# Kernel optimization log

Measured on AMD Instinct MI355X. Metric: run time of the kernel, lower is better.

## Reference

```python
import jax, jax.numpy as jnp
import numpy as np

EPS = 1e-06

def _pairwise_giou(pred, target):
    # pred: [B,P,4], target: [B,G,4] -> gious [B,P,G]
    p = pred[:, :, None, :]   # [B,P,1,4]
    t = target[:, None, :, :] # [B,1,G,4]
    pw = jnp.clip(p[..., 2] - p[..., 0] + 1.0, 0.0)
    ph = jnp.clip(p[..., 3] - p[..., 1] + 1.0, 0.0)
    tw = jnp.clip(t[..., 2] - t[..., 0] + 1.0, 0.0)
    th = jnp.clip(t[..., 3] - t[..., 1] + 1.0, 0.0)
    pred_areas = pw * ph
    target_areas = tw * th
    ix1 = jnp.maximum(p[..., 0], t[..., 0])
    iy1 = jnp.maximum(p[..., 1], t[..., 1])
    ix2 = jnp.minimum(p[..., 2], t[..., 2])
    iy2 = jnp.minimum(p[..., 3], t[..., 3])
    iw = jnp.clip(ix2 - ix1 + 1.0, 0.0)
    ih = jnp.clip(iy2 - iy1 + 1.0, 0.0)
    inter = iw * ih
    unions = pred_areas + target_areas - inter
    ious = jnp.maximum(inter / unions, EPS)
    ox1 = jnp.minimum(p[..., 0], t[..., 0])
    oy1 = jnp.minimum(p[..., 1], t[..., 1])
    ox2 = jnp.maximum(p[..., 2], t[..., 2])
    oy2 = jnp.maximum(p[..., 3], t[..., 3])
    ow = jnp.clip(ox2 - ox1 + 1.0, 0.0)
    oh = jnp.clip(oy2 - oy1 + 1.0, 0.0)
    outer = ow * oh
    gious = ious - (outer - unions) / outer
    return jnp.clip(gious, -1.0, 1.0)


def setup_inputs() -> dict:
    key = jax.random.key(0)
    k1, k2, k3, k4, k5 = jax.random.split(key, 5)
    B, P, G = 32, 2048, 512
    IMG = 1024.0
    # gt boxes: [B,G,4] with x1<=x2, y1<=y2
    gxy = jax.random.uniform(k1, (B, G, 2), dtype=jnp.float32) * (IMG - 64.0)
    gwh = jax.random.uniform(k2, (B, G, 2), dtype=jnp.float32) * 64.0 + 1.0
    imgs_box = jnp.concatenate([gxy, gxy + gwh], axis=-1)
    # pred boxes: [B,P,4]
    pxy = jax.random.uniform(k3, (B, P, 2), dtype=jnp.float32) * (IMG - 64.0)
    pwh = jax.random.uniform(k4, (B, P, 2), dtype=jnp.float32) * 64.0 + 1.0
    pre_BOX = jnp.concatenate([pxy, pxy + pwh], axis=-1)
    labels = jax.random.randint(k5, (B,), 0, 10, dtype=jnp.int64 if jax.config.jax_enable_x64 else jnp.int32)
    return {"imgs_box": imgs_box, "pre_BOX": pre_BOX, "labels": labels}


def reference(imgs_box, pre_BOX, labels):
    B = labels.shape[0]
    gious = _pairwise_giou(pre_BOX, imgs_box)      # [B,P,G]
    max_giou = jnp.max(gious, axis=-1)             # [B,P]
    batch_loss = jnp.sum(1.0 - max_giou)
    return batch_loss / B
```

## Files before the change

### kernel.cpp

```cpp
#include <hip/hip_runtime.h>


constexpr int NP = 2;
constexpr int NW = 8;

__global__ __launch_bounds__(512) void giou_partial_kernel(
    const float4* __restrict__ tgt,
    const float4* __restrict__ pred,
    float* __restrict__ partial,
    int P, int G)
{
    __shared__ float4 sT[512];
    __shared__ float  sA[512];
    __shared__ float  sM[NP * 512];

    const int b    = blockIdx.y;
    const int tid  = threadIdx.x;
    const int lane = tid & 63;
    const int wid  = tid >> 6;

    for (int g = tid; g < G; g += 512) {
        float4 t = tgt[b * G + g];
        t.z += 1.0f; t.w += 1.0f;
        sT[g] = t;
        sA[g] = (t.z - t.x) * (t.w - t.y);
    }
    __syncthreads();

    const int p0 = blockIdx.x * (NP * 64) + lane;
    float4 pb[NP]; float pw[NP], ph[NP], pa[NP];
    #pragma unroll
    for (int k = 0; k < NP; ++k) {
        float4 v = pred[b * P + min(p0 + 64 * k, P - 1)];
        v.z += 1.0f; v.w += 1.0f;
        pb[k] = v;
        pw[k] = v.z - v.x;
        ph[k] = v.w - v.y;
        pa[k] = pw[k] * ph[k];
    }

    const int gq = (G + NW - 1) / NW;
    const int g0 = wid * gq;
    const int g1 = min(g0 + gq, G);

    float numM[NP], denM[NP];
    #pragma unroll
    for (int k = 0; k < NP; ++k) { numM[k] = 0.0f; denM[k] = 1.0f; }

    #pragma unroll 2
    for (int g = g0; g < g1; ++g) {
        const float4 t  = sT[g];
        const float  ta = sA[g];
        const float  tw = t.z - t.x;
        const float  th = t.w - t.y;
        #pragma unroll
        for (int k = 0; k < NP; ++k) {
            float iwr = fminf(pb[k].z, t.z) - fmaxf(pb[k].x, t.x);
            float ihr = fminf(pb[k].w, t.w) - fmaxf(pb[k].y, t.y);
            float inter = fmaxf(iwr, 0.0f) * fmaxf(ihr, 0.0f);
            float un  = (pa[k] + ta) - inter;
            float ow  = (pw[k] + tw) - iwr;
            float oh  = (ph[k] + th) - ihr;
            float outer = ow * oh;
            float num = __builtin_fmaf(un, un, inter * outer);
            float den = un * outer;
            bool better = num * denM[k] > numM[k] * den;
            numM[k] = better ? num : numM[k];
            denM[k] = better ? den : denM[k];
        }
    }

    #pragma unroll
    for (int k = 0; k < NP; ++k)
        sM[k * 512 + tid] = numM[k] * __builtin_amdgcn_rcpf(denM[k]);
    __syncthreads();

    if (wid == 0) {
        float v = 0.0f;
        #pragma unroll
        for (int k = 0; k < NP; ++k) {
            float mm = sM[k * 512 + lane];
            #pragma unroll
            for (int w = 1; w < NW; ++w) mm = fmaxf(mm, sM[k * 512 + w * 64 + lane]);
            v += (p0 + 64 * k < P) ? (2.0f - mm) : 0.0f;
        }
        #pragma unroll
        for (int off = 32; off > 0; off >>= 1)
            v += __shfl_down(v, off, 64);
        if (lane == 0)
            partial[blockIdx.y * gridDim.x + blockIdx.x] = v;
    }
}

__global__ __launch_bounds__(256) void giou_reduce_kernel(
    const float* __restrict__ partial, float* __restrict__ out, int n, float invB)
{
    const int tid = threadIdx.x;
    float v = 0.0f;
    for (int i = tid; i < n; i += 256) v += partial[i];

    #pragma unroll
    for (int off = 32; off > 0; off >>= 1)
        v += __shfl_down(v, off, 64);

    __shared__ float sW[4];
    const int wid = tid >> 6;
    if ((tid & 63) == 0) sW[wid] = v;
    __syncthreads();
    if (tid == 0)
        out[0] = (sW[0] + sW[1] + sW[2] + sW[3]) * invB;
}

extern "C" void kernel_launch(void* const* d_in, const int* in_sizes, int n_in,
                              void* d_out, int out_size, void* d_ws, size_t ws_size,
                              hipStream_t stream) {
    const float* imgs_box = (const float*)d_in[0];
    const float* pre_box  = (const float*)d_in[1];

    const int B = in_sizes[2];
    const int G = in_sizes[0] / (4 * B);
    const int P = in_sizes[1] / (4 * B);

    float* partial = (float*)d_ws;

    const int pblocks = (P + NP * 64 - 1) / (NP * 64);
    dim3 grid(pblocks, B);
    giou_partial_kernel<<<grid, 512, 0, stream>>>(
        (const float4*)imgs_box, (const float4*)pre_box, partial, P, G);

    const int n = pblocks * B;
    giou_reduce_kernel<<<1, 256, 0, stream>>>(partial, (float*)d_out, n, 1.0f / (float)B);
}
```

Baseline: 30.84 us.

## Hold GT boxes in registers and reduce per-pred max with DPP

Restructures the work split so each lane keeps 8 target boxes in registers, covering all 512 GT boxes per wave. Each wave now walks 8 predictions, and the max over GT boxes is reduced across lanes with DPP row shifts and broadcasts. This removes the per-iteration LDS reads of target boxes and the cross-wave shared-memory max, and launches more, smaller blocks. In exchange it adds a cross-lane reduction and a reciprocal per prediction. It also assumes G is at most TPL*64, so correctness depends on the problem shape.

```diff
diff --git a/kernel.cpp b/kernel.cpp
--- a/kernel.cpp
+++ b/kernel.cpp
@@ -1,94 +1,98 @@
 #include <hip/hip_runtime.h>
 
 
-constexpr int NP = 2;
-constexpr int NW = 8;
+constexpr int TPL = 8;
+constexpr int PPW = 8;
+constexpr int NW  = 8;
 
-__global__ __launch_bounds__(512) void giou_partial_kernel(
+template <int CTRL>
+__device__ __forceinline__ float dppmax(float x) {
+    int i = __float_as_int(x);
+    int m = __builtin_amdgcn_update_dpp(i, i, CTRL, 0xF, 0xF, false);
+    return fmaxf(x, __int_as_float(m));
+}
+
+__global__ __launch_bounds__(512, 4) void giou_partial_kernel(
     const float4* __restrict__ tgt,
     const float4* __restrict__ pred,
     float* __restrict__ partial,
     int P, int G)
 {
-    __shared__ float4 sT[512];
-    __shared__ float  sA[512];
-    __shared__ float  sM[NP * 512];
+    __shared__ float4 sP[NW * PPW];
+    __shared__ float  sOut[NW];
 
     const int b    = blockIdx.y;
     const int tid  = threadIdx.x;
     const int lane = tid & 63;
     const int wid  = tid >> 6;
 
-    for (int g = tid; g < G; g += 512) {
-        float4 t = tgt[b * G + g];
-        t.z += 1.0f; t.w += 1.0f;
-        sT[g] = t;
-        sA[g] = (t.z - t.x) * (t.w - t.y);
+    if (tid < NW * PPW) {
+        int pi = blockIdx.x * (NW * PPW) + tid;
+        float4 v = pred[b * P + min(pi, P - 1)];
+        v.z += 1.0f; v.w += 1.0f;
+        sP[tid] = v;
+    }
+
+    float tx1[TPL], ty1[TPL], tx2[TPL], ty2[TPL];
+    #pragma unroll
+    for (int j = 0; j < TPL; ++j) {
+        float4 t = tgt[b * G + min(j * 64 + lane, G - 1)];
+        tx1[j] = t.x; ty1[j] = t.y;
+        tx2[j] = t.z + 1.0f; ty2[j] = t.w + 1.0f;
     }
     __syncthreads();
 
-    const int p0 = blockIdx.x * (NP * 64) + lane;
-    float4 pb[NP]; float pw[NP], ph[NP], pa[NP];
-    #pragma unroll
-    for (int k = 0; k < NP; ++k) {
-        float4 v = pred[b * P + min(p0 + 64 * k, P - 1)];
-        v.z += 1.0f; v.w += 1.0f;
-        pb[k] = v;
-        pw[k] = v.z - v.x;
-        ph[k] = v.w - v.y;
-        pa[k] = pw[k] * ph[k];
-    }
+    float acc = 0.0f;
 
-    const int gq = (G + NW - 1) / NW;
-    const int g0 = wid * gq;
-    const int g1 = min(g0 + gq, G);
+    for (int q = 0; q < PPW; ++q) {
+        const int   pidx = blockIdx.x * (NW * PPW) + wid * PPW + q;
+        const float4 pbx = sP[wid * PPW + q];
+        const float pw = pbx.z - pbx.x;
+        const float ph = pbx.w - pbx.y;
+        const float pa = pw * ph;
 
-    float numM[NP], denM[NP];
-    #pragma unroll
-    for (int k = 0; k < NP; ++k) { numM[k] = 0.0f; denM[k] = 1.0f; }
+        float numM = 0.0f, denM = 1.0f;
 
-    #pragma unroll 2
-    for (int g = g0; g < g1; ++g) {
-        const float4 t  = sT[g];
-        const float  ta = sA[g];
-        const float  tw = t.z - t.x;
-        const float  th = t.w - t.y;
         #pragma unroll
-        for (int k = 0; k < NP; ++k) {
-            float iwr = fminf(pb[k].z, t.z) - fmaxf(pb[k].x, t.x);
-            float ihr = fminf(pb[k].w, t.w) - fmaxf(pb[k].y, t.y);
+        for (int j = 0; j < TPL; ++j) {
+            float tw  = tx2[j] - tx1[j];
+            float th  = ty2[j] - ty1[j];
+            float ta  = tw * th;
+            float iwr = fminf(pbx.z, tx2[j]) - fmaxf(pbx.x, tx1[j]);
+            float ihr = fminf(pbx.w, ty2[j]) - fmaxf(pbx.y, ty1[j]);
             float inter = fmaxf(iwr, 0.0f) * fmaxf(ihr, 0.0f);
-            float un  = (pa[k] + ta) - inter;
-            float ow  = (pw[k] + tw) - iwr;
-            float oh  = (ph[k] + th) - ihr;
+            float un  = (pa + ta) - inter;
+            float ow  = (pw + tw) - iwr;
+            float oh  = (ph + th) - ihr;
             float outer = ow * oh;
             float num = __builtin_fmaf(un, un, inter * outer);
             float den = un * outer;
-            bool better = num * denM[k] > numM[k] * den;
-            numM[k] = better ? num : numM[k];
-            denM[k] = better ? den : denM[k];
+            bool better = num * denM > numM * den;
+            numM = better ? num : numM;
+            denM = better ? den : denM;
         }
+
+        float gi = numM * __builtin_amdgcn_rcpf(denM);
+
+        gi = dppmax<0x111>(gi);
+        gi = dppmax<0x112>(gi);
+        gi = dppmax<0x114>(gi);
+        gi = dppmax<0x118>(gi);
+        gi = dppmax<0x142>(gi);
+        gi = dppmax<0x143>(gi);
+
+        if (lane == 63 && pidx < P)
+            acc += 2.0f - gi;
     }
 
-    #pragma unroll
-    for (int k = 0; k < NP; ++k)
-        sM[k * 512 + tid] = numM[k] * __builtin_amdgcn_rcpf(denM[k]);
+    if (lane == 63) sOut[wid] = acc;
     __syncthreads();
 
-    if (wid == 0) {
+    if (tid == 0) {
         float v = 0.0f;
         #pragma unroll
-        for (int k = 0; k < NP; ++k) {
-            float mm = sM[k * 512 + lane];
-            #pragma unroll
-            for (int w = 1; w < NW; ++w) mm = fmaxf(mm, sM[k * 512 + w * 64 + lane]);
-            v += (p0 + 64 * k < P) ? (2.0f - mm) : 0.0f;
-        }
-        #pragma unroll
-        for (int off = 32; off > 0; off >>= 1)
-            v += __shfl_down(v, off, 64);
-        if (lane == 0)
-            partial[blockIdx.y * gridDim.x + blockIdx.x] = v;
+        for (int w = 0; w < NW; ++w) v += sOut[w];
+        partial[blockIdx.y * gridDim.x + blockIdx.x] = v;
     }
 }
 
@@ -123,7 +127,7 @@
 
     float* partial = (float*)d_ws;
 
-    const int pblocks = (P + NP * 64 - 1) / (NP * 64);
+    const int pblocks = (P + NW * PPW - 1) / (NW * PPW);
     dim3 grid(pblocks, B);
     giou_partial_kernel<<<grid, 512, 0, stream>>>(
         (const float4*)imgs_box, (const float4*)pre_box, partial, P, G);
```

Result: slower. 34.31 us (+11.3%).

## Split G across grid z-dimension and compute GIoU directly with reciprocals

Applied to the files above, without the earlier changes.

Adds a third grid dimension that splits the ground-truth boxes into two halves. Each block writes per-prediction maxima to workspace, and a multi-block reduce kernel combines the halves and accumulates the loss with atomicAdd after a memset. The inner loop drops the cross-multiplied num/den comparison and computes GIoU with two hardware reciprocals plus fmax, and it software-prefetches the next target boxes from LDS. This trades more blocks and an extra workspace round-trip for more parallelism and cheaper inner-loop arithmetic, at the cost of approximate reciprocal precision.

```diff
diff --git a/kernel.cpp b/kernel.cpp
--- a/kernel.cpp
+++ b/kernel.cpp
@@ -3,112 +3,129 @@
 
 constexpr int NP = 2;
 constexpr int NW = 8;
+constexpr int NZ = 2;
+constexpr int GCAP = 1024;
 
-__global__ __launch_bounds__(512) void giou_partial_kernel(
+__global__ __launch_bounds__(512, 8) void giou_max_kernel(
     const float4* __restrict__ tgt,
     const float4* __restrict__ pred,
-    float* __restrict__ partial,
+    float* __restrict__ maxM,
     int P, int G)
 {
-    __shared__ float4 sT[512];
-    __shared__ float  sA[512];
-    __shared__ float  sM[NP * 512];
+    __shared__ float4 sT[GCAP + 2];
+    __shared__ float  sA[GCAP + 2];
+    __shared__ float  sEx[NP][512];
 
-    const int b    = blockIdx.y;
-    const int tid  = threadIdx.x;
-    const int lane = tid & 63;
-    const int wid  = tid >> 6;
+    const int b = blockIdx.y, z = blockIdx.z;
+    const int tid = threadIdx.x, lane = tid & 63, wid = tid >> 6;
 
-    for (int g = tid; g < G; g += 512) {
-        float4 t = tgt[b * G + g];
+    const int Gz  = (G + NZ - 1) / NZ;
+    const int zlo = z * Gz;
+    const int cnt = min(Gz, G - zlo);
+    const int CL  = min(cnt, GCAP);
+
+    for (int i = tid; i < CL; i += 512) {
+        float4 t = tgt[(size_t)b * G + zlo + i];
         t.z += 1.0f; t.w += 1.0f;
-        sT[g] = t;
-        sA[g] = (t.z - t.x) * (t.w - t.y);
+        sT[i] = t;
+        sA[i] = (t.z - t.x) * (t.w - t.y);
+    }
+    if (tid < 2) {
+        sT[CL + tid] = make_float4(0.f, 0.f, 1.f, 1.f);
+        sA[CL + tid] = 1.0f;
+    }
+
+    const int base = blockIdx.x * (NP * 64);
+    float4 pb[NP]; float pw[NP], ph[NP], pa[NP];
+    #pragma unroll
+    for (int k = 0; k < NP; ++k) {
+        float4 v = pred[(size_t)b * P + min(base + 64 * k + lane, P - 1)];
+        v.z += 1.0f; v.w += 1.0f;
+        pb[k] = v; pw[k] = v.z - v.x; ph[k] = v.w - v.y; pa[k] = pw[k] * ph[k];
     }
     __syncthreads();
 
-    const int p0 = blockIdx.x * (NP * 64) + lane;
-    float4 pb[NP]; float pw[NP], ph[NP], pa[NP];
-    #pragma unroll
-    for (int k = 0; k < NP; ++k) {
-        float4 v = pred[b * P + min(p0 + 64 * k, P - 1)];
-        v.z += 1.0f; v.w += 1.0f;
-        pb[k] = v;
-        pw[k] = v.z - v.x;
-        ph[k] = v.w - v.y;
-        pa[k] = pw[k] * ph[k];
-    }
+    const int gq = (CL + NW - 1) / NW;
+    const int g0 = wid * gq;
+    const int g1 = min(g0 + gq, CL);
 
-    const int gq = (G + NW - 1) / NW;
-    const int g0 = wid * gq;
-    const int g1 = min(g0 + gq, G);
+    float m[NP] = {0.0f, 0.0f};
 
-    float numM[NP], denM[NP];
-    #pragma unroll
-    for (int k = 0; k < NP; ++k) { numM[k] = 0.0f; denM[k] = 1.0f; }
+    float4 t0 = sT[g0], t1 = sT[g0 + 1];
+    float  a0 = sA[g0], a1 = sA[g0 + 1];
 
     #pragma unroll 2
     for (int g = g0; g < g1; ++g) {
-        const float4 t  = sT[g];
-        const float  ta = sA[g];
-        const float  tw = t.z - t.x;
-        const float  th = t.w - t.y;
+        float4 t2 = sT[g + 2];
+        float  a2 = sA[g + 2];
+        const float tw = t0.z - t0.x, th = t0.w - t0.y;
+        #pragma unroll
+        for (int k = 0; k < NP; ++k) {
+            float iwr = fminf(pb[k].z, t0.z) - fmaxf(pb[k].x, t0.x);
+            float ihr = fminf(pb[k].w, t0.w) - fmaxf(pb[k].y, t0.y);
+            float inter = fmaxf(iwr, 0.0f) * fmaxf(ihr, 0.0f);
+            float un = (pa[k] + a0) - inter;
+            float outer = ((pw[k] + tw) - iwr) * ((ph[k] + th) - ihr);
+            float gi = __builtin_fmaf(un, __builtin_amdgcn_rcpf(outer),
+                                      inter * __builtin_amdgcn_rcpf(un));
+            m[k] = fmaxf(m[k], gi);
+        }
+        t0 = t1; a0 = a1; t1 = t2; a1 = a2;
+    }
+
+    for (int g = GCAP + wid; g < cnt; g += NW) {
+        float4 t = tgt[(size_t)b * G + zlo + g];
+        t.z += 1.0f; t.w += 1.0f;
+        float ta = (t.z - t.x) * (t.w - t.y);
+        const float tw = t.z - t.x, th = t.w - t.y;
         #pragma unroll
         for (int k = 0; k < NP; ++k) {
             float iwr = fminf(pb[k].z, t.z) - fmaxf(pb[k].x, t.x);
             float ihr = fminf(pb[k].w, t.w) - fmaxf(pb[k].y, t.y);
             float inter = fmaxf(iwr, 0.0f) * fmaxf(ihr, 0.0f);
-            float un  = (pa[k] + ta) - inter;
-            float ow  = (pw[k] + tw) - iwr;
-            float oh  = (ph[k] + th) - ihr;
-            float outer = ow * oh;
-            float num = __builtin_fmaf(un, un, inter * outer);
-            float den = un * outer;
-            bool better = num * denM[k] > numM[k] * den;
-            numM[k] = better ? num : numM[k];
-            denM[k] = better ? den : denM[k];
+            float un = (pa[k] + ta) - inter;
+            float outer = ((pw[k] + tw) - iwr) * ((ph[k] + th) - ihr);
+            float gi = __builtin_fmaf(un, __builtin_amdgcn_rcpf(outer),
+                                      inter * __builtin_amdgcn_rcpf(un));
+            m[k] = fmaxf(m[k], gi);
         }
     }
 
-    #pragma unroll
-    for (int k = 0; k < NP; ++k)
-        sM[k * 512 + tid] = numM[k] * __builtin_amdgcn_rcpf(denM[k]);
+    sEx[0][tid] = m[0]; sEx[1][tid] = m[1];
     __syncthreads();
 
     if (wid == 0) {
-        float v = 0.0f;
         #pragma unroll
         for (int k = 0; k < NP; ++k) {
-            float mm = sM[k * 512 + lane];
+            float mm = sEx[k][lane];
             #pragma unroll
-            for (int w = 1; w < NW; ++w) mm = fmaxf(mm, sM[k * 512 + w * 64 + lane]);
-            v += (p0 + 64 * k < P) ? (2.0f - mm) : 0.0f;
+            for (int w = 1; w < NW; ++w) mm = fmaxf(mm, sEx[k][w * 64 + lane]);
+            int p = base + 64 * k + lane;
+            if (p < P)
+                maxM[((size_t)z * gridDim.y + b) * P + p] = mm;
         }
-        #pragma unroll
-        for (int off = 32; off > 0; off >>= 1)
-            v += __shfl_down(v, off, 64);
-        if (lane == 0)
-            partial[blockIdx.y * gridDim.x + blockIdx.x] = v;
     }
 }
 
 __global__ __launch_bounds__(256) void giou_reduce_kernel(
-    const float* __restrict__ partial, float* __restrict__ out, int n, float invB)
+    const float* __restrict__ maxM, float* __restrict__ out,
+    int n, int nz, float invB)
 {
     const int tid = threadIdx.x;
     float v = 0.0f;
-    for (int i = tid; i < n; i += 256) v += partial[i];
-
+    for (int i = blockIdx.x * 256 + tid; i < n; i += gridDim.x * 256) {
+        float mm = maxM[i];
+        for (int z = 1; z < nz; ++z) mm = fmaxf(mm, maxM[(size_t)z * n + i]);
+        v += 2.0f - mm;
+    }
     #pragma unroll
-    for (int off = 32; off > 0; off >>= 1)
-        v += __shfl_down(v, off, 64);
-
+    for (int off = 32; off > 0; off >>= 1) v += __shfl_down(v, off, 64);
     __shared__ float sW[4];
     const int wid = tid >> 6;
     if ((tid & 63) == 0) sW[wid] = v;
     __syncthreads();
     if (tid == 0)
-        out[0] = (sW[0] + sW[1] + sW[2] + sW[3]) * invB;
+        atomicAdd(out, (sW[0] + sW[1] + sW[2] + sW[3]) * invB);
 }
 
 extern "C" void kernel_launch(void* const* d_in, const int* in_sizes, int n_in,
@@ -116,18 +133,20 @@
                               hipStream_t stream) {
     const float* imgs_box = (const float*)d_in[0];
     const float* pre_box  = (const float*)d_in[1];
-
     const int B = in_sizes[2];
     const int G = in_sizes[0] / (4 * B);
     const int P = in_sizes[1] / (4 * B);
 
-    float* partial = (float*)d_ws;
+    float* maxM = (float*)d_ws;
+
+    hipMemsetAsync(d_out, 0, sizeof(float), stream);
 
     const int pblocks = (P + NP * 64 - 1) / (NP * 64);
-    dim3 grid(pblocks, B);
-    giou_partial_kernel<<<grid, 512, 0, stream>>>(
-        (const float4*)imgs_box, (const float4*)pre_box, partial, P, G);
+    dim3 grid(pblocks, B, NZ);
+    giou_max_kernel<<<grid, 512, 0, stream>>>(
+        (const float4*)imgs_box, (const float4*)pre_box, maxM, P, G);
 
-    const int n = pblocks * B;
-    giou_reduce_kernel<<<1, 256, 0, stream>>>(partial, (float*)d_out, n, 1.0f / (float)B);
+    const int n = B * P;
+    giou_reduce_kernel<<<64, 256, 0, stream>>>(
+        maxM, (float*)d_out, n, NZ, 1.0f / (float)B);
 }
```

New measurement: 34.88 us. 1.13x slower.
